# Kernel optimization log

Hardware: AMD Instinct MI355X
Metric: run time of the kernel (lower is better)

Reference implementation:

```python
import jax, jax.numpy as jnp
import numpy as np

NH = 16  # n_heads

def setup_inputs() -> dict:
    key = jax.random.key(0)
    ks = jax.random.split(key, 5)
    B, T, D = 2, 2048, 2048
    scale = 0.02
    return {
        "x": jax.random.normal(ks[0], (B, T, D), dtype=jnp.float32),
        "Wq": jax.random.normal(ks[1], (D, D), dtype=jnp.float32) * scale,
        "Wk": jax.random.normal(ks[2], (D, D), dtype=jnp.float32) * scale,
        "Wv": jax.random.normal(ks[3], (D, D), dtype=jnp.float32) * scale,
        "Wo": jax.random.normal(ks[4], (D, D), dtype=jnp.float32) * scale,
    }

def reference(x, Wq, Wk, Wv, Wo):
    B, T, D = x.shape
    hd = D // NH
    # torch nn.Linear(d,d,bias=False): y = x @ W.T
    q = (x @ Wq.T).reshape(B, T, NH, hd).transpose(0, 2, 1, 3)  # [B,H,T,hd]
    k = (x @ Wk.T).reshape(B, T, NH, hd).transpose(0, 2, 1, 3)
    v = (x @ Wv.T).reshape(B, T, NH, hd).transpose(0, 2, 1, 3)
    att = jnp.einsum('bhtd,bhsd->bhts', q, k) / jnp.sqrt(jnp.asarray(hd, x.dtype))
    neg = jnp.finfo(att.dtype).min
    mask = jnp.triu(jnp.full((T, T), neg, dtype=att.dtype), k=1)  # causal
    att = att + mask
    w = jax.nn.softmax(att, axis=-1)
    z = jnp.einsum('bhts,bhsd->bhtd', w, v)  # [B,H,T,hd]
    z = z.transpose(0, 2, 1, 3).reshape(B, T, D)
    return z @ Wo.T
```

## Files before the change

### kernel.cpp

```cpp
#include <hip/hip_runtime.h>
#include <hip/hip_bf16.h>
#include <math.h>


typedef __attribute__((ext_vector_type(4))) float  f32x4;
typedef __attribute__((ext_vector_type(8))) __bf16 bf16x8;

union Pack8 { __bf16 h[8]; uint4 u; };
union Pack4 { __bf16 h[4]; uint2 u; };

__device__ __forceinline__ void async16(const void* g, void* l) {
    __builtin_amdgcn_global_load_lds((const __attribute__((address_space(1))) void*)g,
                                     (__attribute__((address_space(3))) void*)l, 16, 0, 0);
}

struct CvtArgs { const float* s[5]; __bf16* d[5]; };

__global__ __launch_bounds__(256) void cvt_all(CvtArgs a) {
    int i = blockIdx.x * 256 + threadIdx.x;
    int t, off;
    if (i < (1 << 20)) { t = 0; off = i; }
    else { int j = i - (1 << 20); t = 1 + (j >> 19); off = j & ((1 << 19) - 1); }
    const float4* s = (const float4*)a.s[t] + (size_t)off * 2;
    float4 f0 = s[0], f1 = s[1];
    Pack8 pk;
    pk.h[0] = (__bf16)f0.x; pk.h[1] = (__bf16)f0.y;
    pk.h[2] = (__bf16)f0.z; pk.h[3] = (__bf16)f0.w;
    pk.h[4] = (__bf16)f1.x; pk.h[5] = (__bf16)f1.y;
    pk.h[6] = (__bf16)f1.z; pk.h[7] = (__bf16)f1.w;
    ((uint4*)a.d[t])[off] = pk.u;
}

__global__ __launch_bounds__(256) void gemm_qkv(const __bf16* __restrict__ A,
        const __bf16* __restrict__ Wq, const __bf16* __restrict__ Wk,
        const __bf16* __restrict__ Wv,
        __bf16* __restrict__ Qo, __bf16* __restrict__ Ko, __bf16* __restrict__ Vt) {
    constexpr int K = 2048, N = 2048, MT = 4096;
    __shared__ __bf16 lds[2][16 * 512];
    const int tid  = threadIdx.x;
    const int w    = tid >> 6;
    const int lane = tid & 63;
    const int lm   = lane & 15;
    const int quad = lane >> 4;
    const int seg  = blockIdx.x >> 4;
    const int col0 = (blockIdx.x & 15) * 128;
    const int row0 = blockIdx.y * 128;
    const __bf16* B = (seg == 0) ? Wq : (seg == 1) ? Wk : Wv;
    const int mw = (w >> 1) * 4;
    const int nw = (w & 1) * 4;

    const __bf16* gA0 = A + (size_t)(row0 + (2 * w) * 16 + lm) * K + quad * 8;
    const __bf16* gA1 = A + (size_t)(row0 + (2 * w + 1) * 16 + lm) * K + quad * 8;
    const __bf16* gB0 = B + (size_t)(col0 + (2 * w) * 16 + lm) * K + quad * 8;
    const __bf16* gB1 = B + (size_t)(col0 + (2 * w + 1) * 16 + lm) * K + quad * 8;

    f32x4 acc[4][4] = {};

#define QKV_ISSUE(k0, buf)                                             \
    do {                                                               \
        async16(gA0 + (k0), lds[buf] + (2 * w) * 512);                 \
        async16(gA1 + (k0), lds[buf] + (2 * w + 1) * 512);             \
        async16(gB0 + (k0), lds[buf] + (8 + 2 * w) * 512);             \
        async16(gB1 + (k0), lds[buf] + (8 + 2 * w + 1) * 512);         \
    } while (0)

#define QKV_COMPUTE(buf)                                               \
    do {                                                               \
        bf16x8 af[4], bfv[4];                                          \
        _Pragma("unroll")                                              \
        for (int mt = 0; mt < 4; ++mt)                                 \
            af[mt] = *(const bf16x8*)(lds[buf] + (mw + mt) * 512 + lane * 8); \
        _Pragma("unroll")                                              \
        for (int nt = 0; nt < 4; ++nt)                                 \
            bfv[nt] = *(const bf16x8*)(lds[buf] + (8 + nw + nt) * 512 + lane * 8); \
        _Pragma("unroll")                                              \
        for (int mt = 0; mt < 4; ++mt)                                 \
            _Pragma("unroll")                                          \
            for (int nt = 0; nt < 4; ++nt)                             \
                acc[mt][nt] = __builtin_amdgcn_mfma_f32_16x16x32_bf16( \
                    af[mt], bfv[nt], acc[mt][nt], 0, 0, 0);            \
    } while (0)

    QKV_ISSUE(0, 0);
    for (int k0 = 0; k0 < K; k0 += 64) {
        __syncthreads();
        QKV_ISSUE(k0 + 32, 1);
        QKV_COMPUTE(0);
        __syncthreads();
        if (k0 + 64 < K) QKV_ISSUE(k0 + 64, 0);
        QKV_COMPUTE(1);
    }
#undef QKV_ISSUE
#undef QKV_COMPUTE

    if (seg < 2) {
        __bf16* C = seg ? Ko : Qo;
#pragma unroll
        for (int mt = 0; mt < 4; ++mt)
#pragma unroll
            for (int nt = 0; nt < 4; ++nt)
#pragma unroll
                for (int r = 0; r < 4; ++r)
                    C[(size_t)(row0 + (mw + mt) * 16 + quad * 4 + r) * N +
                      col0 + (nw + nt) * 16 + lm] = (__bf16)acc[mt][nt][r];
    } else {
#pragma unroll
        for (int mt = 0; mt < 4; ++mt)
#pragma unroll
            for (int nt = 0; nt < 4; ++nt) {
                Pack4 p;
#pragma unroll
                for (int r = 0; r < 4; ++r) p.h[r] = (__bf16)acc[mt][nt][r];
                *(uint2*)&Vt[(size_t)(col0 + (nw + nt) * 16 + lm) * MT +
                             row0 + (mw + mt) * 16 + quad * 4] = p.u;
            }
    }
}

__global__ __launch_bounds__(256) void gemm_wo(const __bf16* __restrict__ A,
                                               const __bf16* __restrict__ B,
                                               float* __restrict__ C) {
    constexpr int K = 2048, N = 2048;
    __shared__ __bf16 lds[2][16 * 512];
    const int tid  = threadIdx.x;
    const int w    = tid >> 6;
    const int lane = tid & 63;
    const int lm   = lane & 15;
    const int quad = lane >> 4;
    const int row0 = blockIdx.y * 128;
    const int col0 = blockIdx.x * 128;
    const int mw   = (w >> 1) * 4;
    const int nw   = (w & 1) * 4;

    const __bf16* gA0 = A + (size_t)(row0 + (2 * w) * 16 + lm) * K + quad * 8;
    const __bf16* gA1 = A + (size_t)(row0 + (2 * w + 1) * 16 + lm) * K + quad * 8;
    const __bf16* gB0 = B + (size_t)(col0 + (2 * w) * 16 + lm) * K + quad * 8;
    const __bf16* gB1 = B + (size_t)(col0 + (2 * w + 1) * 16 + lm) * K + quad * 8;

    f32x4 acc[4][4] = {};

#define WO_ISSUE(k0, buf)                                              \
    do {                                                               \
        async16(gA0 + (k0), lds[buf] + (2 * w) * 512);                 \
        async16(gA1 + (k0), lds[buf] + (2 * w + 1) * 512);             \
        async16(gB0 + (k0), lds[buf] + (8 + 2 * w) * 512);             \
        async16(gB1 + (k0), lds[buf] + (8 + 2 * w + 1) * 512);         \
    } while (0)

#define WO_COMPUTE(buf)                                                \
    do {                                                               \
        bf16x8 af[4], bfv[4];                                          \
        _Pragma("unroll")                                              \
        for (int mt = 0; mt < 4; ++mt)                                 \
            af[mt] = *(const bf16x8*)(lds[buf] + (mw + mt) * 512 + lane * 8); \
        _Pragma("unroll")                                              \
        for (int nt = 0; nt < 4; ++nt)                                 \
            bfv[nt] = *(const bf16x8*)(lds[buf] + (8 + nw + nt) * 512 + lane * 8); \
        _Pragma("unroll")                                              \
        for (int mt = 0; mt < 4; ++mt)                                 \
            _Pragma("unroll")                                          \
            for (int nt = 0; nt < 4; ++nt)                             \
                acc[mt][nt] = __builtin_amdgcn_mfma_f32_16x16x32_bf16( \
                    af[mt], bfv[nt], acc[mt][nt], 0, 0, 0);            \
    } while (0)

    WO_ISSUE(0, 0);
    for (int k0 = 0; k0 < K; k0 += 64) {
        __syncthreads();
        WO_ISSUE(k0 + 32, 1);
        WO_COMPUTE(0);
        __syncthreads();
        if (k0 + 64 < K) WO_ISSUE(k0 + 64, 0);
        WO_COMPUTE(1);
    }
#undef WO_ISSUE
#undef WO_COMPUTE

#pragma unroll
    for (int mt = 0; mt < 4; ++mt)
#pragma unroll
        for (int nt = 0; nt < 4; ++nt)
#pragma unroll
            for (int r = 0; r < 4; ++r)
                C[(size_t)(row0 + (mw + mt) * 16 + quad * 4 + r) * N +
                  col0 + (nw + nt) * 16 + lm] = acc[mt][nt][r];
}

__global__ __launch_bounds__(256) void attn6(const __bf16* __restrict__ Q,
                                             const __bf16* __restrict__ K,
                                             const __bf16* __restrict__ Vt,
                                             __bf16* __restrict__ Z) {
    constexpr int T = 2048, D = 2048, MT = 4096, PS = 72;
    __shared__ __bf16 KVf[2][32 * 512];
    __shared__ __bf16 Pf[4 * 16 * PS];
    const int tid  = threadIdx.x;
    const int w    = tid >> 6;
    const int lane = tid & 63;
    const int lm   = lane & 15;
    const int quad = lane >> 4;
    const int f    = blockIdx.x;
    const int bh   = ((f >> 7) << 3) | (f & 7);
    const int pair = (f >> 3) & 15;
    const int b    = bh >> 4;
    const int h    = bh & 15;

    const size_t qkbase = (size_t)b * T * D + (size_t)h * 128;
    const __bf16* Qh = Q + qkbase;
    const __bf16* Kh = K + qkbase;
    const __bf16* Vh = Vt + (size_t)(h * 128) * MT + (size_t)b * T;
    __bf16* Zh = Z + qkbase;

    bf16x8 ones;
#pragma unroll
    for (int i = 0; i < 8; ++i) ones[i] = (__bf16)1.0f;

    const float c = 0.08838834764831845f;
    __bf16* pw = Pf + w * (16 * PS);

#define ATTN_ISSUE(kv0, buf)                                                     \
    do {                                                                         \
        _Pragma("unroll")                                                        \
        for (int i = 0; i < 4; ++i) {                                            \
            const int fk = w * 4 + i;                                            \
            const int nt = fk >> 2, kk = fk & 3;                                 \
            async16(Kh + (size_t)((kv0) + nt * 16 + lm) * D + kk * 32 + quad * 8,\
                    KVf[buf] + fk * 512);                                        \
            const int on = fk >> 1, kc = fk & 1;                                 \
            async16(Vh + (size_t)(on * 16 + lm) * MT + (kv0) + kc * 32 + quad * 8,\
                    KVf[buf] + (16 + fk) * 512);                                 \
        }                                                                        \
    } while (0)

    for (int ph = 0; ph < 2; ++ph) {
        const int j  = ph ? 31 - pair : pair;
        const int q0 = j * 64 + w * 16;

        bf16x8 qf[4];
#pragma unroll
        for (int kk = 0; kk < 4; ++kk)
            qf[kk] = *(const bf16x8*)(Qh + (size_t)(q0 + lm) * D + kk * 32 + quad * 8);

        f32x4 o[8] = {};
        f32x4 osum = {};

        __syncthreads();
        ATTN_ISSUE(0, 0);
        int buf = 0;

        for (int t = 0; t <= j; ++t) {
            __syncthreads();
            if (t < j) ATTN_ISSUE((t + 1) * 64, buf ^ 1);
            const __bf16* Kc = KVf[buf];
            const __bf16* Vc = KVf[buf] + 16 * 512;
            buf ^= 1;
            const int kv0 = t * 64;

            f32x4 s[4] = {};
#pragma unroll
            for (int nt = 0; nt < 4; ++nt)
#pragma unroll
                for (int kk = 0; kk < 4; ++kk) {
                    bf16x8 kfr = *(const bf16x8*)(Kc + (nt * 4 + kk) * 512 + lane * 8);
                    s[nt] = __builtin_amdgcn_mfma_f32_16x16x32_bf16(qf[kk], kfr, s[nt], 0, 0, 0);
                }

            const bool diag = (t == j);
#pragma unroll
            for (int nt = 0; nt < 4; ++nt)
#pragma unroll
                for (int r = 0; r < 4; ++r) {
                    float v = s[nt][r];
                    if (diag && (kv0 + nt * 16 + lm > q0 + quad * 4 + r)) v = -1e30f;
                    s[nt][r] = __expf(fmaf(v, c, -4.0f));
                }

#pragma unroll
            for (int nt = 0; nt < 4; ++nt)
#pragma unroll
                for (int r = 0; r < 4; ++r)
                    pw[(quad * 4 + r) * PS + nt * 16 + lm] = (__bf16)s[nt][r];

            bf16x8 pf[2];
#pragma unroll
            for (int kc = 0; kc < 2; ++kc)
                pf[kc] = *(const bf16x8*)(pw + lm * PS + kc * 32 + quad * 8);

#pragma unroll
            for (int kc = 0; kc < 2; ++kc) {
                osum = __builtin_amdgcn_mfma_f32_16x16x32_bf16(pf[kc], ones, osum, 0, 0, 0);
#pragma unroll
                for (int on = 0; on < 8; ++on) {
                    bf16x8 vf = *(const bf16x8*)(Vc + (on * 2 + kc) * 512 + lane * 8);
                    o[on] = __builtin_amdgcn_mfma_f32_16x16x32_bf16(pf[kc], vf, o[on], 0, 0, 0);
                }
            }
        }

        float inv[4];
#pragma unroll
        for (int r = 0; r < 4; ++r) inv[r] = 1.f / osum[r];
#pragma unroll
        for (int on = 0; on < 8; ++on)
#pragma unroll
            for (int r = 0; r < 4; ++r)
                Zh[(size_t)(q0 + quad * 4 + r) * D + on * 16 + lm] =
                    (__bf16)(o[on][r] * inv[r]);
    }
#undef ATTN_ISSUE
}

extern "C" void kernel_launch(void* const* d_in, const int* in_sizes, int n_in,
                              void* d_out, int out_size, void* d_ws, size_t ws_size,
                              hipStream_t stream) {
    const float* x  = (const float*)d_in[0];
    const float* Wq = (const float*)d_in[1];
    const float* Wk = (const float*)d_in[2];
    const float* Wv = (const float*)d_in[3];
    const float* Wo = (const float*)d_in[4];
    const int D = 2048, M = 4096;
    const size_t SZ_X = (size_t)M * D;
    const size_t SZ_W = (size_t)D * D;

    __bf16* xb  = (__bf16*)d_ws;
    __bf16* Wqb = xb + SZ_X;
    __bf16* Wkb = Wqb + SZ_W;
    __bf16* Wvb = Wkb + SZ_W;
    __bf16* Wob = Wvb + SZ_W;
    __bf16* Qb  = Wob + SZ_W;
    __bf16* Kb  = Qb + SZ_X;
    __bf16* Vtb = Kb + SZ_X;
    __bf16* Zb  = xb;

    CvtArgs ca;
    ca.s[0] = x;  ca.s[1] = Wq;  ca.s[2] = Wk;  ca.s[3] = Wv;  ca.s[4] = Wo;
    ca.d[0] = xb; ca.d[1] = Wqb; ca.d[2] = Wkb; ca.d[3] = Wvb; ca.d[4] = Wob;
    cvt_all<<<12288, 256, 0, stream>>>(ca);

    gemm_qkv<<<dim3(48, 32), 256, 0, stream>>>(xb, Wqb, Wkb, Wvb, Qb, Kb, Vtb);

    attn6<<<512, 256, 0, stream>>>(Qb, Kb, Vtb, Zb);

    gemm_wo<<<dim3(16, 32), 256, 0, stream>>>(Zb, Wob, (float*)d_out);
}
```

Before: 457.5 us.

## Rewrite QKV GEMM with 256x256 tiles, 8 waves, and staged prefetch pipeline

Reworks the fused QKV projection GEMM from 128x128 tiles with 4 waves to 256x256 tiles with 8 waves per block. Each wave now owns a 128x64 output region. K-step 64 tiles are double-buffered in LDS and the next-next tile is loaded in four pieces interleaved between MFMA quarter-steps, with explicit vmcnt waits, barriers and s_setprio around the MFMA bursts. The goal is higher arithmetic intensity per LDS/global load and better overlap of loads with matrix math, at the cost of 128KB of LDS, high register pressure from 32 accumulators per wave, and only 384 blocks.

```diff
diff --git a/kernel.cpp b/kernel.cpp
--- a/kernel.cpp
+++ b/kernel.cpp
@@ -31,88 +31,146 @@
     ((uint4*)a.d[t])[off] = pk.u;
 }
 
-__global__ __launch_bounds__(256) void gemm_qkv(const __bf16* __restrict__ A,
+__global__ __launch_bounds__(512, 2) void gemm_qkv(const __bf16* __restrict__ A,
         const __bf16* __restrict__ Wq, const __bf16* __restrict__ Wk,
         const __bf16* __restrict__ Wv,
         __bf16* __restrict__ Qo, __bf16* __restrict__ Ko, __bf16* __restrict__ Vt) {
-    constexpr int K = 2048, N = 2048, MT = 4096;
-    __shared__ __bf16 lds[2][16 * 512];
+    constexpr int K = 2048, N = 2048, MT = 4096, NT = K / 64;
+    __shared__ __bf16 lds[2][32768];
     const int tid  = threadIdx.x;
     const int w    = tid >> 6;
     const int lane = tid & 63;
     const int lm   = lane & 15;
     const int quad = lane >> 4;
-    const int seg  = blockIdx.x >> 4;
-    const int col0 = (blockIdx.x & 15) * 128;
-    const int row0 = blockIdx.y * 128;
+    const int wm   = w >> 2;
+    const int wn   = w & 3;
+
+    const int bid   = blockIdx.x;
+    const int seg   = bid >> 7;
+    const int mt    = (bid >> 3) & 15;
+    const int nt    = bid & 7;
+    const int mrow0 = mt * 256;
+    const int ncol0 = nt * 256;
     const __bf16* B = (seg == 0) ? Wq : (seg == 1) ? Wk : Wv;
-    const int mw = (w >> 1) * 4;
-    const int nw = (w & 1) * 4;
-
-    const __bf16* gA0 = A + (size_t)(row0 + (2 * w) * 16 + lm) * K + quad * 8;
-    const __bf16* gA1 = A + (size_t)(row0 + (2 * w + 1) * 16 + lm) * K + quad * 8;
-    const __bf16* gB0 = B + (size_t)(col0 + (2 * w) * 16 + lm) * K + quad * 8;
-    const __bf16* gB1 = B + (size_t)(col0 + (2 * w + 1) * 16 + lm) * K + quad * 8;
-
-    f32x4 acc[4][4] = {};
-
-#define QKV_ISSUE(k0, buf)                                             \
-    do {                                                               \
-        async16(gA0 + (k0), lds[buf] + (2 * w) * 512);                 \
-        async16(gA1 + (k0), lds[buf] + (2 * w + 1) * 512);             \
-        async16(gB0 + (k0), lds[buf] + (8 + 2 * w) * 512);             \
-        async16(gB1 + (k0), lds[buf] + (8 + 2 * w + 1) * 512);         \
-    } while (0)
-
-#define QKV_COMPUTE(buf)                                               \
-    do {                                                               \
-        bf16x8 af[4], bfv[4];                                          \
-        _Pragma("unroll")                                              \
-        for (int mt = 0; mt < 4; ++mt)                                 \
-            af[mt] = *(const bf16x8*)(lds[buf] + (mw + mt) * 512 + lane * 8); \
-        _Pragma("unroll")                                              \
-        for (int nt = 0; nt < 4; ++nt)                                 \
-            bfv[nt] = *(const bf16x8*)(lds[buf] + (8 + nw + nt) * 512 + lane * 8); \
-        _Pragma("unroll")                                              \
-        for (int mt = 0; mt < 4; ++mt)                                 \
-            _Pragma("unroll")                                          \
-            for (int nt = 0; nt < 4; ++nt)                             \
-                acc[mt][nt] = __builtin_amdgcn_mfma_f32_16x16x32_bf16( \
-                    af[mt], bfv[nt], acc[mt][nt], 0, 0, 0);            \
-    } while (0)
-
-    QKV_ISSUE(0, 0);
-    for (int k0 = 0; k0 < K; k0 += 64) {
-        __syncthreads();
-        QKV_ISSUE(k0 + 32, 1);
-        QKV_COMPUTE(0);
-        __syncthreads();
-        if (k0 + 64 < K) QKV_ISSUE(k0 + 64, 0);
-        QKV_COMPUTE(1);
+
+    const int fmA0 = ((w >= 4) ? 8 : 0) + (w & 3);
+    const int fnB0 = ((w >> 1) << 2) | (w & 1);
+    const __bf16* gA0 = A + (size_t)(mrow0 + fmA0 * 16 + lm) * K + quad * 8;
+    const __bf16* gA1 = gA0 + (size_t)64 * K;
+    const __bf16* gB0 = B + (size_t)(ncol0 + fnB0 * 16 + lm) * K + quad * 8;
+    const __bf16* gB1 = gB0 + (size_t)32 * K;
+
+    f32x4  acc[8][4] = {};
+    bf16x8 ra0[4][2], ra1[4][2], rb0[2][2], rb1[2][2];
+
+#define STAGE_A0(t_, bufp_) do {                                            \
+        async16(gA0 + (size_t)(t_) * 64,      (bufp_) + fmA0 * 1024);       \
+        async16(gA0 + (size_t)(t_) * 64 + 32, (bufp_) + fmA0 * 1024 + 512); \
+    } while (0)
+#define STAGE_A1(t_, bufp_) do {                                                  \
+        async16(gA1 + (size_t)(t_) * 64,      (bufp_) + (fmA0 + 4) * 1024);       \
+        async16(gA1 + (size_t)(t_) * 64 + 32, (bufp_) + (fmA0 + 4) * 1024 + 512); \
+    } while (0)
+#define STAGE_B0(t_, bufp_) do {                                                    \
+        async16(gB0 + (size_t)(t_) * 64,      (bufp_) + 16384 + fnB0 * 1024);       \
+        async16(gB0 + (size_t)(t_) * 64 + 32, (bufp_) + 16384 + fnB0 * 1024 + 512); \
+    } while (0)
+#define STAGE_B1(t_, bufp_) do {                                                          \
+        async16(gB1 + (size_t)(t_) * 64,      (bufp_) + 16384 + (fnB0 + 2) * 1024);       \
+        async16(gB1 + (size_t)(t_) * 64 + 32, (bufp_) + 16384 + (fnB0 + 2) * 1024 + 512); \
+    } while (0)
+
+#define READ_A(dst, bufp_, mh) do {                                              \
+        const __bf16* ap_ = (bufp_) + wm * 8192 + (mh) * 4096;                   \
+        _Pragma("unroll") for (int i_ = 0; i_ < 4; ++i_)                         \
+        _Pragma("unroll") for (int kf_ = 0; kf_ < 2; ++kf_)                      \
+            dst[i_][kf_] = *(const bf16x8*)(ap_ + i_ * 1024 + kf_ * 512 + lane * 8); \
+    } while (0)
+#define READ_B(dst, bufp_, nh) do {                                              \
+        const __bf16* bp_ = (bufp_) + 16384 + wn * 4096 + (nh) * 2048;           \
+        _Pragma("unroll") for (int j_ = 0; j_ < 2; ++j_)                         \
+        _Pragma("unroll") for (int kf_ = 0; kf_ < 2; ++kf_)                      \
+            dst[j_][kf_] = *(const bf16x8*)(bp_ + j_ * 1024 + kf_ * 512 + lane * 8); \
+    } while (0)
+#define MMA(mh, nh, Ar, Br) do {                                                 \
+        __builtin_amdgcn_s_setprio(1);                                           \
+        _Pragma("unroll") for (int kf_ = 0; kf_ < 2; ++kf_)                      \
+        _Pragma("unroll") for (int i_ = 0; i_ < 4; ++i_)                         \
+        _Pragma("unroll") for (int j_ = 0; j_ < 2; ++j_)                         \
+            acc[(mh) * 4 + i_][(nh) * 2 + j_] =                                  \
+                __builtin_amdgcn_mfma_f32_16x16x32_bf16(                         \
+                    Ar[i_][kf_], Br[j_][kf_],                                    \
+                    acc[(mh) * 4 + i_][(nh) * 2 + j_], 0, 0, 0);                 \
+        __builtin_amdgcn_s_setprio(0);                                           \
+    } while (0)
+
+    {
+        __bf16* b0p = &lds[0][0];
+        __bf16* b1p = &lds[0][0] + 32768;
+        STAGE_B0(0, b0p); STAGE_A0(0, b0p); STAGE_A1(0, b0p); STAGE_B1(0, b0p);
+        STAGE_B0(1, b1p); STAGE_A0(1, b1p); STAGE_A1(1, b1p); STAGE_B1(1, b1p);
+        asm volatile("s_waitcnt vmcnt(8)" ::: "memory");
+        __builtin_amdgcn_s_barrier();
     }
-#undef QKV_ISSUE
-#undef QKV_COMPUTE
-
+
+    for (int t = 0; t < NT; ++t) {
+        __bf16* bufp = &lds[0][0] + (size_t)(t & 1) * 32768;
+        const bool st = (t + 2 < NT);
+        READ_A(ra0, bufp, 0);
+        READ_B(rb0, bufp, 0);
+        __builtin_amdgcn_s_barrier();
+        MMA(0, 0, ra0, rb0);
+        __builtin_amdgcn_s_barrier();
+        READ_A(ra1, bufp, 1);
+        if (st) { STAGE_B0(t + 2, bufp); STAGE_A0(t + 2, bufp); }
+        __builtin_amdgcn_s_barrier();
+        MMA(1, 0, ra1, rb0);
+        __builtin_amdgcn_s_barrier();
+        READ_B(rb1, bufp, 1);
+        if (st) STAGE_A1(t + 2, bufp);
+        __builtin_amdgcn_s_barrier();
+        MMA(0, 1, ra0, rb1);
+        __builtin_amdgcn_s_barrier();
+        if (st) {
+            asm volatile("s_waitcnt vmcnt(6)" ::: "memory");
+            STAGE_B1(t + 2, bufp);
+        } else {
+            asm volatile("s_waitcnt vmcnt(0)" ::: "memory");
+        }
+        __builtin_amdgcn_s_barrier();
+        MMA(1, 1, ra1, rb1);
+        __builtin_amdgcn_s_barrier();
+    }
+#undef STAGE_A0
+#undef STAGE_A1
+#undef STAGE_B0
+#undef STAGE_B1
+#undef READ_A
+#undef READ_B
+#undef MMA
+
+    const int wrow = mrow0 + wm * 128;
+    const int wcol = ncol0 + wn * 64;
     if (seg < 2) {
         __bf16* C = seg ? Ko : Qo;
 #pragma unroll
-        for (int mt = 0; mt < 4; ++mt)
-#pragma unroll
-            for (int nt = 0; nt < 4; ++nt)
+        for (int mi = 0; mi < 8; ++mi)
+#pragma unroll
+            for (int nj = 0; nj < 4; ++nj)
 #pragma unroll
                 for (int r = 0; r < 4; ++r)
-                    C[(size_t)(row0 + (mw + mt) * 16 + quad * 4 + r) * N +
-                      col0 + (nw + nt) * 16 + lm] = (__bf16)acc[mt][nt][r];
+                    C[(size_t)(wrow + mi * 16 + quad * 4 + r) * N +
+                      wcol + nj * 16 + lm] = (__bf16)acc[mi][nj][r];
     } else {
 #pragma unroll
-        for (int mt = 0; mt < 4; ++mt)
-#pragma unroll
-            for (int nt = 0; nt < 4; ++nt) {
+        for (int mi = 0; mi < 8; ++mi)
+#pragma unroll
+            for (int nj = 0; nj < 4; ++nj) {
                 Pack4 p;
 #pragma unroll
-                for (int r = 0; r < 4; ++r) p.h[r] = (__bf16)acc[mt][nt][r];
-                *(uint2*)&Vt[(size_t)(col0 + (nw + nt) * 16 + lm) * MT +
-                             row0 + (mw + mt) * 16 + quad * 4] = p.u;
+                for (int r = 0; r < 4; ++r) p.h[r] = (__bf16)acc[mi][nj][r];
+                *(uint2*)&Vt[(size_t)(wcol + nj * 16 + lm) * MT +
+                             wrow + mi * 16 + quad * 4] = p.u;
             }
     }
 }
@@ -336,7 +394,7 @@
     ca.d[0] = xb; ca.d[1] = Wqb; ca.d[2] = Wkb; ca.d[3] = Wvb; ca.d[4] = Wob;
     cvt_all<<<12288, 256, 0, stream>>>(ca);
 
-    gemm_qkv<<<dim3(48, 32), 256, 0, stream>>>(xb, Wqb, Wkb, Wvb, Qb, Kb, Vtb);
+    gemm_qkv<<<384, 512, 0, stream>>>(xb, Wqb, Wkb, Wvb, Qb, Kb, Vtb);
 
     attn6<<<512, 256, 0, stream>>>(Qb, Kb, Vtb, Zb);
 
```

After: 408.8 us. -10.7%, faster.
